# Kernel tuning notes

Measured on AMD Instinct MI355X. Metric: run time of the kernel, lower is better.

The kernel has to match this reference:

```python
import jax, jax.numpy as jnp
import numpy as np

D_MODEL = 1024
N_EXPERTS = 8
TOP_K = 2


def setup_inputs() -> dict:
    key = jax.random.key(0)
    ks = jax.random.split(key, 8)
    d, e = D_MODEL, N_EXPERTS
    s = 1.0 / np.sqrt(d)
    return {
        "x": jax.random.normal(ks[0], (4, 2048, d), dtype=jnp.float32),
        "W_gate": jax.random.uniform(ks[1], (d, e), jnp.float32, -s, s),
        "b_gate": jax.random.uniform(ks[2], (e,), jnp.float32, -s, s),
        "W1": jax.random.uniform(ks[3], (e, d, d), jnp.float32, -s, s),
        "b1": jax.random.uniform(ks[4], (e, d), jnp.float32, -s, s),
        "W2": jax.random.uniform(ks[5], (e, d, d), jnp.float32, -s, s),
        "b2": jax.random.uniform(ks[6], (e, d), jnp.float32, -s, s),
    }


def reference(x, W_gate, b_gate, W1, b1, W2, b2):
    B, T, d = x.shape
    xf = x.reshape(-1, d)  # [N, d], N = B*T
    # gating: raw linear scores, top-k selection; top-k raw scores are the
    # combine weights (original applies no softmax to gate scores)
    scores = xf @ W_gate + b_gate  # [N, E]
    topk_val, topk_idx = jax.lax.top_k(scores, TOP_K)  # [N, K]
    # scatter top-k weights into dense [N, E] combine matrix (indices distinct)
    onehot = jax.nn.one_hot(topk_idx, N_EXPERTS, dtype=xf.dtype)  # [N, K, E]
    w = jnp.einsum("nk,nke->ne", topk_val, onehot)  # [N, E]
    # run every expert MLP densely, then mask-combine (static shapes under jit)
    h = jax.nn.relu(jnp.einsum("nd,edh->neh", xf, W1) + b1)  # [N, E, d]
    y = jnp.einsum("neh,ehd->ned", h, W2) + b2  # [N, E, d]
    out = jnp.einsum("ned,ne->nd", y, w)  # weighted combine over experts
    return out.reshape(B, T, d)
```

## Files before the change

### kernel.cpp

```cpp
#include <hip/hip_runtime.h>
#include <hip/hip_bf16.h>


#define NTOK   8192
#define DM     1024
#define NE     8
#define BM     128
#define NSLOT  (NTOK * 2)
#define PADCAP (NSLOT + NE * BM)
#define MAXTILES (PADCAP / BM)

typedef __attribute__((ext_vector_type(8))) short  bf16x8;
typedef __attribute__((ext_vector_type(4))) float  f32x4;
typedef __attribute__((ext_vector_type(8))) unsigned short u16x8;

__device__ __forceinline__ unsigned short f2bf(float f) {
    union { float f; unsigned u; } v; v.f = f;
    unsigned r = v.u + 0x7fffu + ((v.u >> 16) & 1u);
    return (unsigned short)(r >> 16);
}

__device__ __forceinline__ void load_lds16(const ushort* g, ushort* l) {
    __builtin_amdgcn_global_load_lds(
        (const __attribute__((address_space(1))) unsigned int*)g,
        (__attribute__((address_space(3))) unsigned int*)l,
        16, 0, 0);
}

__global__ __launch_bounds__(256) void k_transpose2(const float* __restrict__ W1,
                                                    const float* __restrict__ W2,
                                                    ushort* __restrict__ w1t,
                                                    ushort* __restrict__ w2t,
                                                    int* __restrict__ counts) {
    int tid = threadIdx.x;
    if (blockIdx.x == 0 && blockIdx.y == 0 && blockIdx.z == 0 && tid < 16)
        counts[tid] = 0;
    int ez = blockIdx.z;
    const float* W = (ez < 8 ? W1 : W2) + (size_t)(ez & 7) * DM * DM;
    ushort* Wt = (ez < 8 ? w1t : w2t) + (size_t)(ez & 7) * DM * DM;
    __shared__ float t[64][65];
    int kt = blockIdx.y * 64, nt = blockIdx.x * 64;
    int r16 = tid >> 4, c4 = (tid & 15) * 4;
#pragma unroll
    for (int p = 0; p < 4; p++) {
        int k = p * 16 + r16;
        float4 v = *(const float4*)&W[(size_t)(kt + k) * DM + nt + c4];
        t[k][c4] = v.x; t[k][c4 + 1] = v.y; t[k][c4 + 2] = v.z; t[k][c4 + 3] = v.w;
    }
    __syncthreads();
    int n = tid >> 2, kb = (tid & 3) * 16;
#pragma unroll
    for (int h = 0; h < 2; h++) {
        int k0 = kb + h * 8;
        u16x8 o;
#pragma unroll
        for (int i = 0; i < 8; i++) o[i] = f2bf(t[k0 + i][n]);
        *(u16x8*)&Wt[(size_t)(nt + n) * DM + kt + k0] = o;
    }
}

__global__ __launch_bounds__(256) void k_gate(const float* __restrict__ x,
                                              const float* __restrict__ Wg,
                                              const float* __restrict__ bg,
                                              ushort* __restrict__ xb,
                                              int* __restrict__ tok_e,
                                              float* __restrict__ tok_w,
                                              int* __restrict__ counts,
                                              float* __restrict__ out,
                                              int* __restrict__ slot_token) {
    __shared__ float wgT[NE][DM];
    __shared__ int cnt[NE];
    int tid = threadIdx.x;
    if (tid < NE) cnt[tid] = 0;
    {
        float4 z4 = {0.f, 0.f, 0.f, 0.f};
        float4* orow = (float4*)(out + (size_t)blockIdx.x * 16 * DM);
#pragma unroll
        for (int i = 0; i < 16; i++) orow[i * 256 + tid] = z4;
        int s0 = blockIdx.x * (PADCAP / 512);
        for (int i = tid; i < PADCAP / 512; i += 256) slot_token[s0 + i] = -1;
    }
    for (int i = tid; i < DM * NE; i += 256) {
        int d = i >> 3, e = i & 7;
        wgT[e][d] = Wg[i];
    }
    __syncthreads();
    int wave = tid >> 6, lane = tid & 63;
    int n0 = (blockIdx.x * 4 + wave) * 4;
    const float4* xr[4];
#pragma unroll
    for (int t = 0; t < 4; t++) xr[t] = (const float4*)(x + (size_t)(n0 + t) * DM);

    float acc[4][NE];
#pragma unroll
    for (int t = 0; t < 4; t++)
#pragma unroll
        for (int e = 0; e < NE; e++) acc[t][e] = 0.f;

#pragma unroll
    for (int j = 0; j < 4; j++) {
        float4 xv[4];
#pragma unroll
        for (int t = 0; t < 4; t++) xv[t] = xr[t][j * 64 + lane];
#pragma unroll
        for (int t = 0; t < 4; t++) {
            ushort4 o;
            o.x = f2bf(xv[t].x); o.y = f2bf(xv[t].y);
            o.z = f2bf(xv[t].z); o.w = f2bf(xv[t].w);
            ((ushort4*)xb)[(size_t)(n0 + t) * (DM / 4) + j * 64 + lane] = o;
        }
#pragma unroll
        for (int e = 0; e < NE; e++) {
            float4 wv = ((const float4*)&wgT[e][0])[j * 64 + lane];
#pragma unroll
            for (int t = 0; t < 4; t++) {
                acc[t][e] += xv[t].x * wv.x + xv[t].y * wv.y
                           + xv[t].z * wv.z + xv[t].w * wv.w;
            }
        }
    }
#pragma unroll
    for (int t = 0; t < 4; t++)
#pragma unroll
        for (int e = 0; e < NE; e++) {
#pragma unroll
            for (int off = 32; off >= 1; off >>= 1)
                acc[t][e] += __shfl_xor(acc[t][e], off);
        }
    if (lane < 4) {
        int t = lane, n = n0 + t;
        float sc[NE];
#pragma unroll
        for (int e = 0; e < NE; e++) sc[e] = acc[t][e] + bg[e];
        int e0 = 0; float v0 = sc[0];
#pragma unroll
        for (int e = 1; e < NE; e++) if (sc[e] > v0) { v0 = sc[e]; e0 = e; }
        int e1 = -1; float v1 = -3.0e38f;
#pragma unroll
        for (int e = 0; e < NE; e++) if (e != e0 && sc[e] > v1) { v1 = sc[e]; e1 = e; }
        tok_e[2 * n] = e0;     tok_w[2 * n] = v0;
        tok_e[2 * n + 1] = e1; tok_w[2 * n + 1] = v1;
        atomicAdd(&cnt[e0], 1);
        atomicAdd(&cnt[e1], 1);
    }
    __syncthreads();
    if (tid < NE) atomicAdd(&counts[tid], cnt[tid]);
}

__global__ __launch_bounds__(256) void k_fillplan(const int* __restrict__ tok_e,
                                                  const float* __restrict__ tok_w,
                                                  const int* __restrict__ counts,
                                                  int* __restrict__ cursor,
                                                  int* __restrict__ slot_token,
                                                  float* __restrict__ slot_w,
                                                  int* __restrict__ tile_e,
                                                  int* __restrict__ tile_b,
                                                  int* __restrict__ ntiles) {
    __shared__ int lcnt[NE], lbase[NE];
    int tid = threadIdx.x;
    if (tid < NE) lcnt[tid] = 0;
    __syncthreads();
    int n = blockIdx.x * 256 + tid;
    int e0 = tok_e[2 * n],     e1 = tok_e[2 * n + 1];
    float w0 = tok_w[2 * n],   w1 = tok_w[2 * n + 1];
    int p0 = atomicAdd(&lcnt[e0], 1);
    int p1 = atomicAdd(&lcnt[e1], 1);
    __syncthreads();
    if (tid < NE) lbase[tid] = atomicAdd(&cursor[tid], lcnt[tid]);
    if (blockIdx.x == 0 && tid == 32) {
        int t = 0, o2 = 0;
        for (int e = 0; e < NE; e++) {
            int nt = (counts[e] + BM - 1) / BM;
            for (int i = 0; i < nt; i++) { tile_e[t] = e; tile_b[t] = o2 + i * BM; t++; }
            o2 += nt * BM;
        }
        *ntiles = t;
    }
    __syncthreads();
    int base[NE]; int off = 0;
#pragma unroll
    for (int e = 0; e < NE; e++) {
        base[e] = off;
        off += ((counts[e] + BM - 1) / BM) * BM;
    }
    int s0 = base[e0] + lbase[e0] + p0;
    slot_token[s0] = n; slot_w[s0] = w0;
    int s1 = base[e1] + lbase[e1] + p1;
    slot_token[s1] = n; slot_w[s1] = w1;
}

template <int PHASE>
__global__ __launch_bounds__(256) void k_gemm(const ushort* __restrict__ A,
                                              const ushort* __restrict__ Wt,
                                              const float* __restrict__ bias,
                                              const int* __restrict__ slot_token,
                                              const float* __restrict__ slot_w,
                                              const int* __restrict__ tile_e,
                                              const int* __restrict__ tile_b,
                                              const int* __restrict__ ntiles,
                                              ushort* __restrict__ Hout,
                                              float* __restrict__ out) {
    int flat = blockIdx.x;
    int wid = (flat & 7) * MAXTILES + (flat >> 3);
    int t = wid >> 3;
    if (t >= *ntiles) return;
    int ncol0 = (wid & 7) << 7;
    int e = tile_e[t];
    int sbase = tile_b[t];

    __shared__ ushort As[3][4096];
    __shared__ ushort Bs[3][4096];

    int tid = threadIdx.x;
    int wave = tid >> 6, lane = tid & 63, quad = lane >> 4, lm = lane & 15;
    int wm = wave >> 1, wn = wave & 1;

    const ushort* Wte = Wt + (size_t)e * DM * DM;

    int sr = lane >> 2;
    int gseg = (lane & 3) ^ ((lane >> 4) & 3);
    const ushort* aptr[2];
    const ushort* bptr[2];
#pragma unroll
    for (int ci = 0; ci < 2; ci++) {
        int row = (wave * 2 + ci) * 16 + sr;
        int ar;
        if (PHASE == 1) {
            ar = slot_token[sbase + row];
            if (ar < 0) ar = 0;
        } else {
            ar = sbase + row;
        }
        aptr[ci] = A + (size_t)ar * DM + gseg * 8;
        bptr[ci] = Wte + (size_t)(ncol0 + row) * DM + gseg * 8;
    }

    f32x4 acc[4][4];
#pragma unroll
    for (int i = 0; i < 4; i++)
#pragma unroll
        for (int j = 0; j < 4; j++) acc[i][j] = (f32x4){0.f, 0.f, 0.f, 0.f};

    int asel = ((quad ^ (lm >> 2)) & 3) * 8;
    int abase = (wm * 64 + lm) * 32 + asel;
    int bbase = (wn * 64 + lm) * 32 + asel;

#define ISSUE(buf, koff)                                          \
    do {                                                          \
        _Pragma("unroll")                                         \
        for (int ci = 0; ci < 2; ci++) {                          \
            int cb = (wave * 2 + ci) * 512;                       \
            load_lds16(aptr[ci] + (koff), &As[(buf)][cb]);        \
            load_lds16(bptr[ci] + (koff), &Bs[(buf)][cb]);        \
        }                                                         \
    } while (0)

#define COMPUTE(buf)                                                          \
    do {                                                                      \
        const ushort* Ab = As[(buf)];                                         \
        const ushort* Bb = Bs[(buf)];                                         \
        bf16x8 av[4], bv[4];                                                  \
        _Pragma("unroll")                                                     \
        for (int f = 0; f < 4; f++) {                                         \
            av[f] = *(const bf16x8*)&Ab[abase + f * 512];                     \
            bv[f] = *(const bf16x8*)&Bb[bbase + f * 512];                     \
        }                                                                     \
        _Pragma("unroll")                                                     \
        for (int fm = 0; fm < 4; fm++)                                        \
            _Pragma("unroll")                                                 \
            for (int fn = 0; fn < 4; fn++)                                    \
                acc[fm][fn] = __builtin_amdgcn_mfma_f32_16x16x32_bf16(        \
                    av[fm], bv[fn], acc[fm][fn], 0, 0, 0);                    \
    } while (0)

    ISSUE(0, 0);
    ISSUE(1, 32);
#pragma unroll 3
    for (int it = 0; it < 30; ++it) {
        ISSUE((it + 2) % 3, (it + 2) * 32);
        __builtin_amdgcn_s_waitcnt(0x0F78);
        __builtin_amdgcn_s_barrier();
        __builtin_amdgcn_sched_barrier(0);
        COMPUTE(it % 3);
        __builtin_amdgcn_sched_barrier(0);
        __builtin_amdgcn_s_waitcnt(0xC07F);
        __builtin_amdgcn_s_barrier();
    }
    __builtin_amdgcn_s_waitcnt(0x0F74);
    __builtin_amdgcn_s_barrier();
    __builtin_amdgcn_sched_barrier(0);
    COMPUTE(0);
    __builtin_amdgcn_sched_barrier(0);
    __builtin_amdgcn_s_waitcnt(0xC07F);
    __builtin_amdgcn_s_barrier();
    __builtin_amdgcn_s_waitcnt(0x0F70);
    __builtin_amdgcn_s_barrier();
    __builtin_amdgcn_sched_barrier(0);
    COMPUTE(1);
#undef ISSUE
#undef COMPUTE

#pragma unroll
    for (int fm = 0; fm < 4; fm++) {
        int rowg = wm * 64 + fm * 16 + quad * 4;
        if (PHASE == 1) {
#pragma unroll
            for (int fn = 0; fn < 4; fn++) {
                int col = ncol0 + wn * 64 + fn * 16 + lm;
                float bv2 = bias[e * DM + col];
#pragma unroll
                for (int r = 0; r < 4; r++) {
                    float v = acc[fm][fn][r] + bv2;
                    v = fmaxf(v, 0.f);
                    Hout[(size_t)(sbase + rowg + r) * DM + col] = f2bf(v);
                }
            }
        } else {
            int tk[4]; float wv[4];
#pragma unroll
            for (int r = 0; r < 4; r++) {
                tk[r] = slot_token[sbase + rowg + r];
                wv[r] = slot_w[sbase + rowg + r];
            }
#pragma unroll
            for (int fn = 0; fn < 4; fn++) {
                int col = ncol0 + wn * 64 + fn * 16 + lm;
                float bv2 = bias[e * DM + col];
#pragma unroll
                for (int r = 0; r < 4; r++) {
                    if (tk[r] >= 0) {
                        float v = wv[r] * (acc[fm][fn][r] + bv2);
                        atomicAdd(&out[(size_t)tk[r] * DM + col], v);
                    }
                }
            }
        }
    }
}

extern "C" void kernel_launch(void* const* d_in, const int* in_sizes, int n_in,
                              void* d_out, int out_size, void* d_ws, size_t ws_size,
                              hipStream_t stream) {
    const float* x  = (const float*)d_in[0];
    const float* Wg = (const float*)d_in[1];
    const float* bg = (const float*)d_in[2];
    const float* W1 = (const float*)d_in[3];
    const float* b1 = (const float*)d_in[4];
    const float* W2 = (const float*)d_in[5];
    const float* b2 = (const float*)d_in[6];
    float* out = (float*)d_out;

    char* ws = (char*)d_ws;
    ushort* xb         = (ushort*)(ws + 0);
    ushort* w1t        = (ushort*)(ws + 16777216);
    ushort* w2t        = (ushort*)(ws + 33554432);
    ushort* H          = (ushort*)(ws + 50331648);
    int*    tok_e      = (int*)  (ws + 85983232);
    float*  tok_w      = (float*)(ws + 86048768);
    int*    slot_token = (int*)  (ws + 86114304);
    float*  slot_w     = (float*)(ws + 86183936);
    int*    counts     = (int*)  (ws + 86253568);
    int*    cursor     = counts + 8;
    int*    tile_e     = counts + 24;
    int*    tile_b     = tile_e + MAXTILES;
    int*    ntiles     = tile_b + MAXTILES;

    dim3 tg(16, 16, 16);
    k_transpose2<<<tg, 256, 0, stream>>>(W1, W2, w1t, w2t, counts);
    k_gate<<<NTOK / 16, 256, 0, stream>>>(x, Wg, bg, xb, tok_e, tok_w, counts,
                                          out, slot_token);
    k_fillplan<<<NTOK / 256, 256, 0, stream>>>(tok_e, tok_w, counts, cursor,
                                               slot_token, slot_w,
                                               tile_e, tile_b, ntiles);

    dim3 gg(8 * MAXTILES);
    k_gemm<1><<<gg, 256, 0, stream>>>(xb, w1t, b1, slot_token, slot_w,
                                      tile_e, tile_b, ntiles, H, nullptr);
    k_gemm<2><<<gg, 256, 0, stream>>>(H, w2t, b2, slot_token, slot_w,
                                      tile_e, tile_b, ntiles, nullptr, out);
}
```

Baseline: 325.4 us.

## Shrink GEMM N-tile to 64, double-buffer LDS, add MFMA priority

The expert GEMM tile narrows from 128x128 to 128x64, which doubles the grid so more workgroups are available per CU. The LDS pipeline drops from triple to double buffering, and s_setprio is raised around the MFMA block. The aim is better occupancy and load balance over the ragged expert tiles. In exchange, each workgroup reuses its A tile less, A-matrix reloads from global memory double, and the shallower prefetch may expose more load latency.

```diff
diff --git a/kernel.cpp b/kernel.cpp
--- a/kernel.cpp
+++ b/kernel.cpp
@@ -201,15 +201,15 @@
                                               ushort* __restrict__ Hout,
                                               float* __restrict__ out) {
     int flat = blockIdx.x;
-    int wid = (flat & 7) * MAXTILES + (flat >> 3);
-    int t = wid >> 3;
+    int wid = (flat & 7) * (MAXTILES * 2) + (flat >> 3);
+    int t = wid >> 4;
     if (t >= *ntiles) return;
-    int ncol0 = (wid & 7) << 7;
+    int ncol0 = (wid & 15) << 6;
     int e = tile_e[t];
     int sbase = tile_b[t];
 
-    __shared__ ushort As[3][4096];
-    __shared__ ushort Bs[3][4096];
+    __shared__ ushort As[2][4096];
+    __shared__ ushort Bs[2][2048];
 
     int tid = threadIdx.x;
     int wave = tid >> 6, lane = tid & 63, quad = lane >> 4, lm = lane & 15;
@@ -220,7 +220,7 @@
     int sr = lane >> 2;
     int gseg = (lane & 3) ^ ((lane >> 4) & 3);
     const ushort* aptr[2];
-    const ushort* bptr[2];
+    const ushort* bptr;
 #pragma unroll
     for (int ci = 0; ci < 2; ci++) {
         int row = (wave * 2 + ci) * 16 + sr;
@@ -232,71 +232,64 @@
             ar = sbase + row;
         }
         aptr[ci] = A + (size_t)ar * DM + gseg * 8;
-        bptr[ci] = Wte + (size_t)(ncol0 + row) * DM + gseg * 8;
-    }
-
-    f32x4 acc[4][4];
+    }
+    {
+        int brow = wave * 16 + sr;
+        bptr = Wte + (size_t)(ncol0 + brow) * DM + gseg * 8;
+    }
+
+    f32x4 acc[4][2];
 #pragma unroll
     for (int i = 0; i < 4; i++)
 #pragma unroll
-        for (int j = 0; j < 4; j++) acc[i][j] = (f32x4){0.f, 0.f, 0.f, 0.f};
+        for (int j = 0; j < 2; j++) acc[i][j] = (f32x4){0.f, 0.f, 0.f, 0.f};
 
     int asel = ((quad ^ (lm >> 2)) & 3) * 8;
     int abase = (wm * 64 + lm) * 32 + asel;
-    int bbase = (wn * 64 + lm) * 32 + asel;
-
-#define ISSUE(buf, koff)                                          \
-    do {                                                          \
-        _Pragma("unroll")                                         \
-        for (int ci = 0; ci < 2; ci++) {                          \
-            int cb = (wave * 2 + ci) * 512;                       \
-            load_lds16(aptr[ci] + (koff), &As[(buf)][cb]);        \
-            load_lds16(bptr[ci] + (koff), &Bs[(buf)][cb]);        \
-        }                                                         \
+    int bbase = (wn * 32 + lm) * 32 + asel;
+
+#define ISSUE(buf, koff)                                              \
+    do {                                                              \
+        load_lds16(aptr[0] + (koff), &As[(buf)][(wave * 2 + 0) * 512]); \
+        load_lds16(aptr[1] + (koff), &As[(buf)][(wave * 2 + 1) * 512]); \
+        load_lds16(bptr + (koff), &Bs[(buf)][wave * 512]);            \
     } while (0)
 
 #define COMPUTE(buf)                                                          \
     do {                                                                      \
         const ushort* Ab = As[(buf)];                                         \
         const ushort* Bb = Bs[(buf)];                                         \
-        bf16x8 av[4], bv[4];                                                  \
+        bf16x8 av[4], bv[2];                                                  \
         _Pragma("unroll")                                                     \
-        for (int f = 0; f < 4; f++) {                                         \
-            av[f] = *(const bf16x8*)&Ab[abase + f * 512];                     \
-            bv[f] = *(const bf16x8*)&Bb[bbase + f * 512];                     \
-        }                                                                     \
+        for (int f = 0; f < 4; f++) av[f] = *(const bf16x8*)&Ab[abase + f * 512]; \
+        _Pragma("unroll")                                                     \
+        for (int f = 0; f < 2; f++) bv[f] = *(const bf16x8*)&Bb[bbase + f * 512]; \
+        __builtin_amdgcn_s_setprio(1);                                        \
         _Pragma("unroll")                                                     \
         for (int fm = 0; fm < 4; fm++)                                        \
             _Pragma("unroll")                                                 \
-            for (int fn = 0; fn < 4; fn++)                                    \
+            for (int fn = 0; fn < 2; fn++)                                    \
                 acc[fm][fn] = __builtin_amdgcn_mfma_f32_16x16x32_bf16(        \
                     av[fm], bv[fn], acc[fm][fn], 0, 0, 0);                    \
+        __builtin_amdgcn_s_setprio(0);                                        \
     } while (0)
 
     ISSUE(0, 0);
-    ISSUE(1, 32);
-#pragma unroll 3
-    for (int it = 0; it < 30; ++it) {
-        ISSUE((it + 2) % 3, (it + 2) * 32);
-        __builtin_amdgcn_s_waitcnt(0x0F78);
+#pragma unroll 2
+    for (int it = 0; it < 32; ++it) {
+        if (it < 31) {
+            ISSUE((it + 1) & 1, (it + 1) * 32);
+            __builtin_amdgcn_s_waitcnt(0x0F73);
+        } else {
+            __builtin_amdgcn_s_waitcnt(0x0F70);
+        }
         __builtin_amdgcn_s_barrier();
         __builtin_amdgcn_sched_barrier(0);
-        COMPUTE(it % 3);
+        COMPUTE(it & 1);
         __builtin_amdgcn_sched_barrier(0);
         __builtin_amdgcn_s_waitcnt(0xC07F);
         __builtin_amdgcn_s_barrier();
     }
-    __builtin_amdgcn_s_waitcnt(0x0F74);
-    __builtin_amdgcn_s_barrier();
-    __builtin_amdgcn_sched_barrier(0);
-    COMPUTE(0);
-    __builtin_amdgcn_sched_barrier(0);
-    __builtin_amdgcn_s_waitcnt(0xC07F);
-    __builtin_amdgcn_s_barrier();
-    __builtin_amdgcn_s_waitcnt(0x0F70);
-    __builtin_amdgcn_s_barrier();
-    __builtin_amdgcn_sched_barrier(0);
-    COMPUTE(1);
 #undef ISSUE
 #undef COMPUTE
 
@@ -305,8 +298,8 @@
         int rowg = wm * 64 + fm * 16 + quad * 4;
         if (PHASE == 1) {
 #pragma unroll
-            for (int fn = 0; fn < 4; fn++) {
-                int col = ncol0 + wn * 64 + fn * 16 + lm;
+            for (int fn = 0; fn < 2; fn++) {
+                int col = ncol0 + wn * 32 + fn * 16 + lm;
                 float bv2 = bias[e * DM + col];
 #pragma unroll
                 for (int r = 0; r < 4; r++) {
@@ -323,8 +316,8 @@
                 wv[r] = slot_w[sbase + rowg + r];
             }
 #pragma unroll
-            for (int fn = 0; fn < 4; fn++) {
-                int col = ncol0 + wn * 64 + fn * 16 + lm;
+            for (int fn = 0; fn < 2; fn++) {
+                int col = ncol0 + wn * 32 + fn * 16 + lm;
                 float bv2 = bias[e * DM + col];
 #pragma unroll
                 for (int r = 0; r < 4; r++) {
@@ -373,7 +366,7 @@
                                                slot_token, slot_w,
                                                tile_e, tile_b, ntiles);
 
-    dim3 gg(8 * MAXTILES);
+    dim3 gg(16 * MAXTILES);
     k_gemm<1><<<gg, 256, 0, stream>>>(xb, w1t, b1, slot_token, slot_w,
                                       tile_e, tile_b, ntiles, H, nullptr);
     k_gemm<2><<<gg, 256, 0, stream>>>(H, w2t, b2, slot_token, slot_w,
```

New measurement: 331.4 us. About the same (+1.9%).
